# Kernel optimization log

Measured on AMD Instinct MI355X. Metric: run time of the kernel, lower is better.

## Reference

```python
import jax, jax.numpy as jnp
import numpy as np

N, FIN, HID, OUT, NC = 4096, 3000, 512, 64, 10


def _xavier(key, shape):
    b = (6.0 / (shape[0] + shape[1])) ** 0.5
    return jax.random.uniform(key, shape, minval=-b, maxval=b, dtype=jnp.float32)


def setup_inputs() -> dict:
    key = jax.random.key(0)
    ks = jax.random.split(key, 12)
    feat = jax.random.normal(ks[0], (N, FIN), jnp.float32)
    feat_a = jax.random.normal(ks[1], (N, FIN), jnp.float32)
    feat_mask = jax.random.normal(ks[2], (N, FIN), jnp.float32)
    adj = jax.random.uniform(ks[3], (N, N), jnp.float32)
    adj = adj / adj.sum(1, keepdims=True)  # row-normalized dense adjacency
    identify_matrix = jnp.eye(N, dtype=jnp.float32)
    graph_neigh = jnp.ones((N, N), jnp.float32)
    w2_1 = _xavier(ks[4], (FIN, HID))
    w2_2 = _xavier(ks[5], (HID, OUT))
    w2 = _xavier(ks[6], (OUT, FIN))
    lamda1 = jax.random.normal(ks[7], (N, 1), jnp.float32) * 0.5
    lamda2 = jax.random.normal(ks[8], (N, 1), jnp.float32) * 0.5
    cluster_w = _xavier(ks[9], (NC, OUT))
    cluster_b = jnp.zeros((NC,), jnp.float32)
    disc_w = _xavier(ks[10], (OUT, OUT)).reshape(1, OUT, OUT)
    disc_b = jnp.zeros((1,), jnp.float32)
    teacher_centers = jnp.zeros((1, OUT), jnp.float32)
    return dict(feat=feat, feat_a=feat_a, feat_mask=feat_mask, adj=adj,
                identify_matrix=identify_matrix, graph_neigh=graph_neigh,
                w2_1=w2_1, w2_2=w2_2, w2=w2, lamda1=lamda1, lamda2=lamda2,
                cluster_w=cluster_w, cluster_b=cluster_b, disc_w=disc_w,
                disc_b=disc_b, teacher_centers=teacher_centers)


def reference(feat, feat_a, feat_mask, adj, identify_matrix, graph_neigh,
              w2_1, w2_2, w2, lamda1, lamda2, cluster_w, cluster_b,
              disc_w, disc_b, teacher_centers):
    relu = jax.nn.relu

    def prop(z):
        # (lamda1 * I + lamda2 * adj) @ z  ==  lamda1 * z + lamda2 * (adj @ z)
        # (identify_matrix is the identity; row-scaling distributes over matmul)
        return lamda1 * z + lamda2 * jnp.matmul(adj, z)

    def branch(x):  # dropout is identity in eval mode
        z = relu(prop(jnp.matmul(x, w2_1)))
        return prop(jnp.matmul(z, w2_2))

    z = branch(feat)
    hiden_emb = z
    h = jnp.matmul(adj, jnp.matmul(z, w2))
    emb = relu(z)
    z_a = branch(feat_a)
    emb_a = relu(z_a)
    z_mask = branch(feat_mask)
    emb_mask = relu(z_mask)

    def readout(e):
        vsum = jnp.matmul(graph_neigh, e)
        g = vsum / graph_neigh.sum(1, keepdims=True)
        g = g / jnp.maximum(jnp.linalg.norm(g, axis=1, keepdims=True), 1e-12)
        return jax.nn.sigmoid(g)

    g, g_a, g_mask = readout(emb), readout(emb_a), readout(emb_mask)

    def disc(c, h_pl, h_mi):  # nn.Bilinear(n_h, n_h, 1); c broadcast to all rows
        sc1 = jnp.einsum('nd,ode,ne->no', h_pl, disc_w, c) + disc_b
        sc2 = jnp.einsum('nd,ode,ne->no', h_mi, disc_w, c) + disc_b
        return jnp.concatenate([sc1, sc2], axis=1)

    ret = disc(g, emb, emb_a)
    ret_a = disc(g_a, emb_a, emb)
    ret_mask = disc(g_mask, emb_mask, emb)

    c = jnp.matmul(z, cluster_w.T) + cluster_b
    c_mask = jnp.matmul(z_mask, cluster_w.T) + cluster_b

    def dino_loss(teacher, student):
        teacher = jax.lax.stop_gradient(teacher)
        sp = jax.nn.softmax(student / 0.9, axis=-1)
        tp = jax.nn.softmax((teacher - teacher_centers) / 0.06, axis=-1)
        return -(tp * jnp.log(sp + 1e-20)).sum(-1).mean()

    loss_mse = (dino_loss(z, z_mask) + dino_loss(z_mask, z)) / 2
    return (hiden_emb, h, ret, ret_a, ret_mask, c, c_mask, loss_mse)
```

## Files before the change

kernel.cpp:

```cpp
#include <hip/hip_runtime.h>
#include <math.h>


typedef __attribute__((ext_vector_type(8))) short bf16x8;
typedef __attribute__((ext_vector_type(4))) float f32x4;

__device__ inline ushort f2bf(float x) {
    unsigned u = __float_as_uint(x);
    return (ushort)((u + 0x7fffu + ((u >> 16) & 1u)) >> 16);
}
__device__ inline float bf2f(ushort h) { return __uint_as_float(((unsigned)h) << 16); }
__device__ inline int swzb(int row, int kb) {
    return ((row << 6) | kb) ^ ((row & 7) << 4);
}

struct SplitPtrs {
    const float*  A[3];
    const ushort* BTh[3];
    const ushort* BTl[3];
    const float*  Y[3];
    float*        C[3];
};

template<int EPI>
__global__ __launch_bounds__(256)
void gemm_mfma(SplitPtrs p, const float* __restrict__ l1, const float* __restrict__ l2,
               int K, int Kpad, int lda, int ldbt, int N) {
    const int zb = blockIdx.z;
    const float*  __restrict__ A   = p.A[zb];
    const ushort* __restrict__ BTh = p.BTh[zb];
    const ushort* __restrict__ BTl = p.BTl[zb];
    const float*  __restrict__ Y   = p.Y[zb];
    float* __restrict__ C = p.C[zb];

    const int tid  = threadIdx.x;
    const int lane = tid & 63;
    const int wave = tid >> 6;
    const int wm = wave >> 1, wn = wave & 1;
    const int lr = lane & 15, lg = lane >> 4;
    const int m0 = blockIdx.y * 128, n0 = blockIdx.x * 128;

    __shared__ ushort As[2][2][4096];
    __shared__ ushort Bs[2][2][4096];

    f32x4 acc[4][4];
#pragma unroll
    for (int i = 0; i < 4; ++i)
#pragma unroll
        for (int j = 0; j < 4; ++j) acc[i][j] = (f32x4){0.f, 0.f, 0.f, 0.f};

    int a_r[4], a_k[4];
#pragma unroll
    for (int p4 = 0; p4 < 4; ++p4) {
        int idx = tid + p4 * 256;
        a_r[p4] = idx >> 3; a_k[p4] = (idx & 7) * 4;
    }
    int b_n[2], b_k[2];
#pragma unroll
    for (int p2 = 0; p2 < 2; ++p2) {
        int idx = tid + p2 * 256;
        b_n[p2] = idx >> 2; b_k[p2] = (idx & 3) * 8;
    }

    float4 areg[4];
    uint4  bhreg[2], blreg[2];

    auto LOAD = [&](int k0) {
#pragma unroll
        for (int p4 = 0; p4 < 4; ++p4) {
            int k = k0 + a_k[p4];
            float4 v = make_float4(0.f, 0.f, 0.f, 0.f);
            if (k < K) v = *(const float4*)(A + (size_t)(m0 + a_r[p4]) * lda + k);
            areg[p4] = v;
        }
#pragma unroll
        for (int p2 = 0; p2 < 2; ++p2) {
            size_t off = (size_t)(n0 + b_n[p2]) * ldbt + k0 + b_k[p2];
            bhreg[p2] = *(const uint4*)(BTh + off);
            blreg[p2] = *(const uint4*)(BTl + off);
        }
    };
    auto WRITE = [&](int buf) {
#pragma unroll
        for (int p4 = 0; p4 < 4; ++p4) {
            float f[4] = {areg[p4].x, areg[p4].y, areg[p4].z, areg[p4].w};
            ushort h[4], l[4];
#pragma unroll
            for (int e = 0; e < 4; ++e) {
                h[e] = f2bf(f[e]);
                l[e] = f2bf(f[e] - bf2f(h[e]));
            }
            int off = swzb(a_r[p4], a_k[p4] * 2);
            *(uint2*)((char*)&As[buf][0][0] + off) =
                make_uint2((unsigned)h[0] | ((unsigned)h[1] << 16),
                           (unsigned)h[2] | ((unsigned)h[3] << 16));
            *(uint2*)((char*)&As[buf][1][0] + off) =
                make_uint2((unsigned)l[0] | ((unsigned)l[1] << 16),
                           (unsigned)l[2] | ((unsigned)l[3] << 16));
        }
#pragma unroll
        for (int p2 = 0; p2 < 2; ++p2) {
            int off = swzb(b_n[p2], b_k[p2] * 2);
            *(uint4*)((char*)&Bs[buf][0][0] + off) = bhreg[p2];
            *(uint4*)((char*)&Bs[buf][1][0] + off) = blreg[p2];
        }
    };

    LOAD(0);
    WRITE(0);
    const int nsteps = Kpad >> 5;
    for (int s = 0; s < nsteps; ++s) {
        const int cur = s & 1;
        if (s + 1 < nsteps) LOAD((s + 1) << 5);
        __syncthreads();
        bf16x8 af[2][4], bfr[2][4];
#pragma unroll
        for (int i = 0; i < 4; ++i) {
            int off = swzb(wm * 64 + i * 16 + lr, lg * 16);
            af[0][i] = *(const bf16x8*)((const char*)&As[cur][0][0] + off);
            af[1][i] = *(const bf16x8*)((const char*)&As[cur][1][0] + off);
        }
#pragma unroll
        for (int j = 0; j < 4; ++j) {
            int off = swzb(wn * 64 + j * 16 + lr, lg * 16);
            bfr[0][j] = *(const bf16x8*)((const char*)&Bs[cur][0][0] + off);
            bfr[1][j] = *(const bf16x8*)((const char*)&Bs[cur][1][0] + off);
        }
#pragma unroll
        for (int i = 0; i < 4; ++i)
#pragma unroll
            for (int j = 0; j < 4; ++j) {
                acc[i][j] = __builtin_amdgcn_mfma_f32_16x16x32_bf16(af[0][i], bfr[0][j], acc[i][j], 0, 0, 0);
                acc[i][j] = __builtin_amdgcn_mfma_f32_16x16x32_bf16(af[0][i], bfr[1][j], acc[i][j], 0, 0, 0);
                acc[i][j] = __builtin_amdgcn_mfma_f32_16x16x32_bf16(af[1][i], bfr[0][j], acc[i][j], 0, 0, 0);
            }
        if (s + 1 < nsteps) WRITE(cur ^ 1);
    }

#pragma unroll
    for (int i = 0; i < 4; ++i) {
#pragma unroll
        for (int r = 0; r < 4; ++r) {
            const int m = m0 + wm * 64 + i * 16 + lg * 4 + r;
            float L1 = 0.f, L2 = 0.f;
            if (EPI == 1) { L1 = l1[m]; L2 = l2[m]; }
#pragma unroll
            for (int j = 0; j < 4; ++j) {
                const int n = n0 + wn * 64 + j * 16 + lr;
                float v = acc[i][j][r];
                if (EPI == 1) {
                    float y = Y[(size_t)m * N + n];
                    v = fmaxf(L1 * y + L2 * v, 0.f);
                }
                C[(size_t)m * N + n] = v;
            }
        }
    }
}

__global__ __launch_bounds__(256)
void gemm_thin(const float* __restrict__ A, int lda,
               const ushort* __restrict__ BTh, const ushort* __restrict__ BTl, int ldbt,
               float* __restrict__ slab, int Mtot, int Nslab, int KC) {
    const int kc = blockIdx.x;
    const int m0 = blockIdx.y * 128;
    const int n0 = blockIdx.z * 64;
    const int tid = threadIdx.x;
    const int lane = tid & 63, wave = tid >> 6;
    const int lr = lane & 15, lg = lane >> 4;

    __shared__ ushort As[2][4096];
    __shared__ ushort Bs[2][2048];

    f32x4 acc[2][4];
#pragma unroll
    for (int i = 0; i < 2; ++i)
#pragma unroll
        for (int j = 0; j < 4; ++j) acc[i][j] = (f32x4){0.f, 0.f, 0.f, 0.f};

    const int kbeg = kc * KC;
    for (int k0 = kbeg; k0 < kbeg + KC; k0 += 32) {
#pragma unroll
        for (int p4 = 0; p4 < 4; ++p4) {
            int idx = tid + p4 * 256;
            int r = idx >> 3, kk = (idx & 7) * 4;
            float4 v = *(const float4*)(A + (size_t)(m0 + r) * lda + k0 + kk);
            float f[4] = {v.x, v.y, v.z, v.w};
            ushort h[4], l[4];
#pragma unroll
            for (int e = 0; e < 4; ++e) {
                h[e] = f2bf(f[e]);
                l[e] = f2bf(f[e] - bf2f(h[e]));
            }
            int off = swzb(r, kk * 2);
            *(uint2*)((char*)&As[0][0] + off) =
                make_uint2((unsigned)h[0] | ((unsigned)h[1] << 16),
                           (unsigned)h[2] | ((unsigned)h[3] << 16));
            *(uint2*)((char*)&As[1][0] + off) =
                make_uint2((unsigned)l[0] | ((unsigned)l[1] << 16),
                           (unsigned)l[2] | ((unsigned)l[3] << 16));
        }
        {
            int n = tid >> 2, kk8 = (tid & 3) * 8;
            size_t soff = (size_t)(n0 + n) * ldbt + k0 + kk8;
            int off = swzb(n, kk8 * 2);
            *(uint4*)((char*)&Bs[0][0] + off) = *(const uint4*)(BTh + soff);
            *(uint4*)((char*)&Bs[1][0] + off) = *(const uint4*)(BTl + soff);
        }
        __syncthreads();
        bf16x8 af[2][2], bfr[2][4];
#pragma unroll
        for (int i = 0; i < 2; ++i) {
            int off = swzb(wave * 32 + i * 16 + lr, lg * 16);
            af[0][i] = *(const bf16x8*)((const char*)&As[0][0] + off);
            af[1][i] = *(const bf16x8*)((const char*)&As[1][0] + off);
        }
#pragma unroll
        for (int j = 0; j < 4; ++j) {
            int off = swzb(j * 16 + lr, lg * 16);
            bfr[0][j] = *(const bf16x8*)((const char*)&Bs[0][0] + off);
            bfr[1][j] = *(const bf16x8*)((const char*)&Bs[1][0] + off);
        }
#pragma unroll
        for (int i = 0; i < 2; ++i)
#pragma unroll
            for (int j = 0; j < 4; ++j) {
                acc[i][j] = __builtin_amdgcn_mfma_f32_16x16x32_bf16(af[0][i], bfr[0][j], acc[i][j], 0, 0, 0);
                acc[i][j] = __builtin_amdgcn_mfma_f32_16x16x32_bf16(af[0][i], bfr[1][j], acc[i][j], 0, 0, 0);
                acc[i][j] = __builtin_amdgcn_mfma_f32_16x16x32_bf16(af[1][i], bfr[0][j], acc[i][j], 0, 0, 0);
            }
        __syncthreads();
    }

    float* out = slab + (size_t)kc * Mtot * Nslab;
#pragma unroll
    for (int i = 0; i < 2; ++i)
#pragma unroll
        for (int r = 0; r < 4; ++r) {
            const int m = m0 + wave * 32 + i * 16 + lg * 4 + r;
#pragma unroll
            for (int j = 0; j < 4; ++j) {
                const int n = n0 + j * 16 + lr;
                out[(size_t)m * Nslab + n] = acc[i][j][r];
            }
        }
}

__global__ void combine_sum(const float* __restrict__ slab, float* __restrict__ C,
                            int E, int nkc) {
    int e = (blockIdx.x * 256 + threadIdx.x) * 4;
    float4 s = make_float4(0.f, 0.f, 0.f, 0.f);
    for (int kc = 0; kc < nkc; ++kc) {
        float4 v = *(const float4*)(slab + (size_t)kc * E + e);
        s.x += v.x; s.y += v.y; s.z += v.z; s.w += v.w;
    }
    *(float4*)(C + e) = s;
}

struct ZOut { float* z[3]; };
__global__ void combine_g4(const float* __restrict__ slab, const float* __restrict__ y2,
                           const float* __restrict__ l1, const float* __restrict__ l2,
                           ZOut zo, int nkc) {
    int idx4 = blockIdx.x * 256 + threadIdx.x;
    int m = idx4 / 48;
    int n = (idx4 % 48) * 4;
    float4 s = make_float4(0.f, 0.f, 0.f, 0.f);
    for (int kc = 0; kc < nkc; ++kc) {
        float4 v = *(const float4*)(slab + (size_t)kc * 786432 + (size_t)m * 192 + n);
        s.x += v.x; s.y += v.y; s.z += v.z; s.w += v.w;
    }
    int b = n >> 6, d = n & 63;
    const float L1 = l1[m], L2 = l2[m];
    float4 y = *(const float4*)(y2 + (size_t)b * 262144 + (size_t)m * 64 + d);
    float4 r = make_float4(L1 * y.x + L2 * s.x, L1 * y.y + L2 * s.y,
                           L1 * y.z + L2 * s.z, L1 * y.w + L2 * s.w);
    *(float4*)(zo.z[b] + (size_t)m * 64 + d) = r;
}

__global__ __launch_bounds__(256)
void convT_split(const float* __restrict__ in, ushort* __restrict__ oh,
                 ushort* __restrict__ ol, int R, int C, int Ks) {
    __shared__ float t[64][65];
    const int r0 = blockIdx.x * 64, c0 = blockIdx.y * 64;
    const float* inz = in + (size_t)blockIdx.z * R * C;
    ushort* ohz = oh + (size_t)blockIdx.z * C * Ks;
    ushort* olz = ol + (size_t)blockIdx.z * C * Ks;
    const int tid = threadIdx.x;
#pragma unroll
    for (int pass = 0; pass < 16; ++pass) {
        int idx = tid + pass * 256;
        int r = idx >> 6, c = idx & 63;
        float v = 0.f;
        if (r0 + r < R) v = inz[(size_t)(r0 + r) * C + c0 + c];
        t[r][c] = v;
    }
    __syncthreads();
#pragma unroll
    for (int pass = 0; pass < 16; ++pass) {
        int idx = tid + pass * 256;
        int c = idx >> 6, r = idx & 63;
        float v = t[r][c];
        ushort h = f2bf(v);
        ushort l = f2bf(v - bf2f(h));
        size_t o = (size_t)(c0 + c) * Ks + r0 + r;
        ohz[o] = h; olz[o] = l;
    }
}

struct Ptrs3 {
    const float* A[3];
    const float* B[3];
    const float* Y[3];
    float*       C[3];
};

__global__ __launch_bounds__(256)
void gemm128(Ptrs3 p, int M, int N, int K) {
    const int zb = blockIdx.z;
    const float* __restrict__ A = p.A[zb];
    const float* __restrict__ B = p.B[zb];
    float* __restrict__ C = p.C[zb];

    const int tid = threadIdx.x;
    const int tm = tid >> 4, tn = tid & 15;
    const int m0 = blockIdx.y * 128, n0 = blockIdx.x * 128;

    __shared__ float As[16][132];
    __shared__ float Bs[16][132];

    float acc[2][2][4][4];
#pragma unroll
    for (int qi = 0; qi < 2; ++qi)
#pragma unroll
        for (int qj = 0; qj < 2; ++qj)
#pragma unroll
            for (int i = 0; i < 4; ++i)
#pragma unroll
                for (int j = 0; j < 4; ++j) acc[qi][qj][i][j] = 0.f;

    for (int k0 = 0; k0 < K; k0 += 16) {
        {
            int idx = tid * 4;
#pragma unroll
            for (int it = 0; it < 2; ++it, idx += 1024) {
                int r = idx >> 4, c = idx & 15;
                int k = k0 + c;
                const float* ap = A + (size_t)(m0 + r) * K + k;
                float4 v = make_float4(0.f, 0.f, 0.f, 0.f);
                if (k + 3 < K) {
                    v = *(const float4*)ap;
                } else {
                    if (k + 0 < K) v.x = ap[0];
                    if (k + 1 < K) v.y = ap[1];
                    if (k + 2 < K) v.z = ap[2];
                }
                As[c + 0][r] = v.x; As[c + 1][r] = v.y;
                As[c + 2][r] = v.z; As[c + 3][r] = v.w;
            }
        }
        {
            int idx = tid * 4;
#pragma unroll
            for (int it = 0; it < 2; ++it, idx += 1024) {
                int r = idx >> 7, c = idx & 127;
                int k = k0 + r, n = n0 + c;
                float4 v = make_float4(0.f, 0.f, 0.f, 0.f);
                if (k < K) {
                    const float* bp = B + (size_t)k * N + n;
                    if (n + 3 < N) {
                        v = *(const float4*)bp;
                    } else {
                        if (n + 0 < N) v.x = bp[0];
                        if (n + 1 < N) v.y = bp[1];
                        if (n + 2 < N) v.z = bp[2];
                    }
                }
                *(float4*)&Bs[r][c] = v;
            }
        }
        __syncthreads();

#pragma unroll
        for (int kk = 0; kk < 16; ++kk) {
            float4 a0 = *(const float4*)&As[kk][tm * 4];
            float4 a1 = *(const float4*)&As[kk][64 + tm * 4];
            float4 b0 = *(const float4*)&Bs[kk][tn * 4];
            float4 b1 = *(const float4*)&Bs[kk][64 + tn * 4];
            float a[2][4] = {{a0.x, a0.y, a0.z, a0.w}, {a1.x, a1.y, a1.z, a1.w}};
            float b[2][4] = {{b0.x, b0.y, b0.z, b0.w}, {b1.x, b1.y, b1.z, b1.w}};
#pragma unroll
            for (int qi = 0; qi < 2; ++qi)
#pragma unroll
                for (int qj = 0; qj < 2; ++qj)
#pragma unroll
                    for (int i = 0; i < 4; ++i)
#pragma unroll
                        for (int j = 0; j < 4; ++j)
                            acc[qi][qj][i][j] = fmaf(a[qi][i], b[qj][j], acc[qi][qj][i][j]);
        }
        __syncthreads();
    }

#pragma unroll
    for (int qi = 0; qi < 2; ++qi)
#pragma unroll
        for (int i = 0; i < 4; ++i) {
            const int m = m0 + qi * 64 + tm * 4 + i;
#pragma unroll
            for (int qj = 0; qj < 2; ++qj) {
                const int n = n0 + qj * 64 + tn * 4;
                float r[4] = {acc[qi][qj][i][0], acc[qi][qj][i][1],
                              acc[qi][qj][i][2], acc[qi][qj][i][3]};
                if (n + 3 < N) {
                    *(float4*)&C[(size_t)m * N + n] = make_float4(r[0], r[1], r[2], r[3]);
                } else {
#pragma unroll
                    for (int e = 0; e < 4; ++e)
                        if (n + e < N) C[(size_t)m * N + n + e] = r[e];
                }
            }
        }
}

__device__ inline float wsum64(float x) {
#pragma unroll
    for (int m = 32; m >= 1; m >>= 1) x += __shfl_xor(x, m);
    return x;
}
__device__ inline float wmax64(float x) {
#pragma unroll
    for (int m = 32; m >= 1; m >>= 1) x = fmaxf(x, __shfl_xor(x, m));
    return x;
}

__global__ void zero_small(float* gsum, float* loss) {
    int t = threadIdx.x;
    if (t < 192) gsum[t] = 0.f;
    if (t == 0) *loss = 0.f;
}

__global__ void colsum_relu(const float* __restrict__ z0,
                            const float* __restrict__ z1,
                            const float* __restrict__ z2,
                            float* __restrict__ gsum) {
    const float* z = blockIdx.y == 0 ? z0 : (blockIdx.y == 1 ? z1 : z2);
    int t = threadIdx.x;
    int col = t & 63, rq = t >> 6;
    int row0 = blockIdx.x * 128;
    float s = 0.f;
    for (int r = rq; r < 128; r += 4)
        s += fmaxf(z[(size_t)(row0 + r) * 64 + col], 0.f);
    __shared__ float red[4][64];
    red[rq][col] = s;
    __syncthreads();
    if (t < 64) {
        float tot = red[0][t] + red[1][t] + red[2][t] + red[3][t];
        atomicAdd(&gsum[blockIdx.y * 64 + t], tot);
    }
}

__global__ void finish_g(const float* __restrict__ gsum,
                         const float* __restrict__ disc_w,
                         float* __restrict__ v) {
    int d = threadIdx.x;
    __shared__ float g[64];
    for (int b = 0; b < 3; ++b) {
        float m = gsum[b * 64 + d] * (1.f / 4096.f);
        float nrm = sqrtf(wsum64(m * m));
        float den = fmaxf(nrm, 1e-12f);
        float gv = 1.f / (1.f + expf(-m / den));
        g[d] = gv;
        __syncthreads();
        float acc = 0.f;
        for (int e = 0; e < 64; ++e) acc += disc_w[d * 64 + e] * g[e];
        v[b * 64 + d] = acc;
        __syncthreads();
    }
}

__global__ void rows_kernel(const float* __restrict__ z,
                            const float* __restrict__ z_a,
                            const float* __restrict__ z_mask,
                            const float* __restrict__ v,
                            const float* __restrict__ disc_b,
                            const float* __restrict__ cw,
                            const float* __restrict__ cb,
                            const float* __restrict__ tc,
                            float* __restrict__ ret,
                            float* __restrict__ ret_a,
                            float* __restrict__ ret_mask,
                            float* __restrict__ c_out,
                            float* __restrict__ c_mask_out,
                            float* __restrict__ loss) {
    int wid = threadIdx.x >> 6;
    int lane = threadIdx.x & 63;
    int row = blockIdx.x * 4 + wid;
    size_t base = (size_t)row * 64 + lane;
    float zf = z[base], za = z_a[base], zm = z_mask[base];
    float ef = fmaxf(zf, 0.f), ea = fmaxf(za, 0.f), em = fmaxf(zm, 0.f);
    float v0 = v[lane], v1 = v[64 + lane], v2 = v[128 + lane];
    float db = disc_b[0];
    float s;
    s = wsum64(ef * v0); if (lane == 0) ret[row * 2 + 0] = s + db;
    s = wsum64(ea * v0); if (lane == 0) ret[row * 2 + 1] = s + db;
    s = wsum64(ea * v1); if (lane == 0) ret_a[row * 2 + 0] = s + db;
    s = wsum64(ef * v1); if (lane == 0) ret_a[row * 2 + 1] = s + db;
    s = wsum64(em * v2); if (lane == 0) ret_mask[row * 2 + 0] = s + db;
    s = wsum64(ef * v2); if (lane == 0) ret_mask[row * 2 + 1] = s + db;
#pragma unroll
    for (int k = 0; k < 10; ++k) {
        float w = cw[k * 64 + lane];
        s = wsum64(zf * w); if (lane == 0) c_out[row * 10 + k] = s + cb[k];
        s = wsum64(zm * w); if (lane == 0) c_mask_out[row * 10 + k] = s + cb[k];
    }
    float tcl = tc[lane];
    float l1v, l2v;
    {
        float x = zm * (1.f / 0.9f);
        float mx = wmax64(x); float pv = expf(x - mx); float sum = wsum64(pv);
        float sp = pv / sum;
        float xt = (zf - tcl) * (1.f / 0.06f);
        float mt = wmax64(xt); float pt = expf(xt - mt); float st = wsum64(pt);
        float tp = pt / st;
        l1v = -wsum64(tp * logf(sp + 1e-20f));
    }
    {
        float x = zf * (1.f / 0.9f);
        float mx = wmax64(x); float pv = expf(x - mx); float sum = wsum64(pv);
        float sp = pv / sum;
        float xt = (zm - tcl) * (1.f / 0.06f);
        float mt = wmax64(xt); float pt = expf(xt - mt); float st = wsum64(pt);
        float tp = pt / st;
        l2v = -wsum64(tp * logf(sp + 1e-20f));
    }
    if (lane == 0) atomicAdd(loss, (l1v + l2v) * (0.5f / 4096.f));
}

extern "C" void kernel_launch(void* const* d_in, const int* in_sizes, int n_in,
                              void* d_out, int out_size, void* d_ws, size_t ws_size,
                              hipStream_t stream) {
    (void)in_sizes; (void)n_in; (void)out_size; (void)ws_size;
    const float* feat   = (const float*)d_in[0];
    const float* feat_a = (const float*)d_in[1];
    const float* feat_m = (const float*)d_in[2];
    const float* adj    = (const float*)d_in[3];
    const float* w2_1   = (const float*)d_in[6];
    const float* w2_2   = (const float*)d_in[7];
    const float* w2     = (const float*)d_in[8];
    const float* l1     = (const float*)d_in[9];
    const float* l2     = (const float*)d_in[10];
    const float* cw     = (const float*)d_in[11];
    const float* cb     = (const float*)d_in[12];
    const float* dw     = (const float*)d_in[13];
    const float* dbv    = (const float*)d_in[14];
    const float* tc     = (const float*)d_in[15];

    float* out      = (float*)d_out;
    float* z_feat   = out;
    float* h_out    = out + 262144;
    float* ret      = out + 262144 + 12288000;
    float* ret_a    = ret + 8192;
    float* ret_mask = ret_a + 8192;
    float* c_out    = ret_mask + 8192;
    float* c_mask   = c_out + 40960;
    float* loss     = c_mask + 40960;

    float* ws = (float*)d_ws;
    size_t o = 0;
    float* y1   = ws + o; o += 6291456;
    float* z1   = ws + o; o += 6291456;
    float* y2   = ws + o; o += 786432;
    float* z_a  = ws + o; o += 262144;
    float* z_m  = ws + o; o += 262144;
    float* u    = ws + o; o += 262144;
    float* gsum = ws + o; o += 256;
    float* vv   = ws + o; o += 256;
    ushort* w21t_h = (ushort*)(ws + o); o += 770048;
    ushort* w21t_l = (ushort*)(ws + o); o += 770048;
    ushort* w22t_h = (ushort*)(ws + o); o += 16384;
    ushort* w22t_l = (ushort*)(ws + o); o += 16384;
    float* y1t_region = ws + o; o += 6291456;
    ushort* y1t_h  = (ushort*)y1t_region;
    ushort* y1t_l  = (ushort*)(y1t_region + 3145728);
    ushort* y2t_h  = (ushort*)y1t_region;
    ushort* y2t_l  = (ushort*)(y1t_region + 393216);
    ushort* zt_h   = (ushort*)(y1t_region + 786432);
    ushort* zt_l   = (ushort*)(y1t_region + 917504);
    float* slab = y1;

    zero_small<<<1, 256, 0, stream>>>(gsum, loss);

    convT_split<<<dim3(47, 8, 1), 256, 0, stream>>>(w2_1, w21t_h, w21t_l, 3000, 512, 3008);
    convT_split<<<dim3(8, 1, 1), 256, 0, stream>>>(w2_2, w22t_h, w22t_l, 512, 64, 512);

    SplitPtrs s1{};
    s1.A[0] = feat; s1.A[1] = feat_a; s1.A[2] = feat_m;
    s1.BTh[0] = s1.BTh[1] = s1.BTh[2] = w21t_h;
    s1.BTl[0] = s1.BTl[1] = s1.BTl[2] = w21t_l;
    s1.C[0] = y1; s1.C[1] = y1 + 2097152; s1.C[2] = y1 + 4194304;
    gemm_mfma<0><<<dim3(4, 32, 3), 256, 0, stream>>>(s1, nullptr, nullptr, 3000, 3008, 3000, 3008, 512);

    convT_split<<<dim3(64, 8, 3), 256, 0, stream>>>(y1, y1t_h, y1t_l, 4096, 512, 4096);

    SplitPtrs s2{};
    s2.A[0] = s2.A[1] = s2.A[2] = adj;
    s2.BTh[0] = y1t_h; s2.BTh[1] = y1t_h + 2097152; s2.BTh[2] = y1t_h + 4194304;
    s2.BTl[0] = y1t_l; s2.BTl[1] = y1t_l + 2097152; s2.BTl[2] = y1t_l + 4194304;
    s2.Y[0] = y1; s2.Y[1] = y1 + 2097152; s2.Y[2] = y1 + 4194304;
    s2.C[0] = z1; s2.C[1] = z1 + 2097152; s2.C[2] = z1 + 4194304;
    gemm_mfma<1><<<dim3(4, 32, 3), 256, 0, stream>>>(s2, l1, l2, 4096, 4096, 4096, 4096, 512);

    gemm_thin<<<dim3(2, 96, 1), 256, 0, stream>>>(z1, 512, w22t_h, w22t_l, 512,
                                                  slab, 12288, 64, 256);
    combine_sum<<<768, 256, 0, stream>>>(slab, y2, 786432, 2);

    convT_split<<<dim3(64, 1, 3), 256, 0, stream>>>(y2, y2t_h, y2t_l, 4096, 64, 4096);

    gemm_thin<<<dim3(8, 32, 3), 256, 0, stream>>>(adj, 4096, y2t_h, y2t_l, 4096,
                                                  slab, 4096, 192, 512);
    ZOut zo{}; zo.z[0] = z_feat; zo.z[1] = z_a; zo.z[2] = z_m;
    combine_g4<<<768, 256, 0, stream>>>(slab, y2, l1, l2, zo, 8);

    convT_split<<<dim3(64, 1, 1), 256, 0, stream>>>(z_feat, zt_h, zt_l, 4096, 64, 4096);

    gemm_thin<<<dim3(8, 32, 1), 256, 0, stream>>>(adj, 4096, zt_h, zt_l, 4096,
                                                  slab, 4096, 64, 512);
    combine_sum<<<256, 256, 0, stream>>>(slab, u, 262144, 8);

    Ptrs3 b6{};
    b6.A[0] = u; b6.B[0] = w2; b6.C[0] = h_out;
    gemm128<<<dim3(24, 32, 1), 256, 0, stream>>>(b6, 4096, 3000, 64);

    colsum_relu<<<dim3(32, 3), 256, 0, stream>>>(z_feat, z_a, z_m, gsum);
    finish_g<<<1, 64, 0, stream>>>(gsum, dw, vv);
    rows_kernel<<<1024, 256, 0, stream>>>(z_feat, z_a, z_m, vv, dbv, cw, cb, tc,
                                          ret, ret_a, ret_mask, c_out, c_mask, loss);
}
```

Baseline: 956.0 us.

## Narrow MFMA GEMM tiles to 128x64, single-buffer LDS, and route final GEMM through MFMA

The split-bf16 MFMA GEMM now uses 128x64 output tiles with a single LDS buffer instead of double buffering, which doubles the grid for the two large GEMMs so more blocks can be resident. The final u@w2 product now runs on the MFMA kernel with a pre-transposed split-bf16 w2 instead of the scalar FP32 gemm128, and convT_split gains column bounds checks to support this. The z1@w2_2 thin GEMM uses a finer K split with more partial slabs. In exchange, B-tile reuse per block drops and the single buffer adds an extra barrier per K step, reducing load/compute overlap.

```diff
diff --git a/kernel.cpp b/kernel.cpp
--- a/kernel.cpp
+++ b/kernel.cpp
@@ -38,16 +38,16 @@
     const int wave = tid >> 6;
     const int wm = wave >> 1, wn = wave & 1;
     const int lr = lane & 15, lg = lane >> 4;
-    const int m0 = blockIdx.y * 128, n0 = blockIdx.x * 128;
-
-    __shared__ ushort As[2][2][4096];
-    __shared__ ushort Bs[2][2][4096];
-
-    f32x4 acc[4][4];
+    const int m0 = blockIdx.y * 128, n0 = blockIdx.x * 64;
+
+    __shared__ ushort As[2][4096];
+    __shared__ ushort Bs[2][2048];
+
+    f32x4 acc[4][2];
 #pragma unroll
     for (int i = 0; i < 4; ++i)
 #pragma unroll
-        for (int j = 0; j < 4; ++j) acc[i][j] = (f32x4){0.f, 0.f, 0.f, 0.f};
+        for (int j = 0; j < 2; ++j) acc[i][j] = (f32x4){0.f, 0.f, 0.f, 0.f};
 
     int a_r[4], a_k[4];
 #pragma unroll
@@ -55,15 +55,10 @@
         int idx = tid + p4 * 256;
         a_r[p4] = idx >> 3; a_k[p4] = (idx & 7) * 4;
     }
-    int b_n[2], b_k[2];
-#pragma unroll
-    for (int p2 = 0; p2 < 2; ++p2) {
-        int idx = tid + p2 * 256;
-        b_n[p2] = idx >> 2; b_k[p2] = (idx & 3) * 8;
-    }
+    const int b_n = tid >> 2, b_k = (tid & 3) * 8;
 
     float4 areg[4];
-    uint4  bhreg[2], blreg[2];
+    uint4  bhreg, blreg;
 
     auto LOAD = [&](int k0) {
 #pragma unroll
@@ -73,14 +68,11 @@
             if (k < K) v = *(const float4*)(A + (size_t)(m0 + a_r[p4]) * lda + k);
             areg[p4] = v;
         }
-#pragma unroll
-        for (int p2 = 0; p2 < 2; ++p2) {
-            size_t off = (size_t)(n0 + b_n[p2]) * ldbt + k0 + b_k[p2];
-            bhreg[p2] = *(const uint4*)(BTh + off);
-            blreg[p2] = *(const uint4*)(BTl + off);
-        }
+        size_t off = (size_t)(n0 + b_n) * ldbt + k0 + b_k;
+        bhreg = *(const uint4*)(BTh + off);
+        blreg = *(const uint4*)(BTl + off);
     };
-    auto WRITE = [&](int buf) {
+    auto WRITE = [&]() {
 #pragma unroll
         for (int p4 = 0; p4 < 4; ++p4) {
             float f[4] = {areg[p4].x, areg[p4].y, areg[p4].z, areg[p4].w};
@@ -91,50 +83,46 @@
                 l[e] = f2bf(f[e] - bf2f(h[e]));
             }
             int off = swzb(a_r[p4], a_k[p4] * 2);
-            *(uint2*)((char*)&As[buf][0][0] + off) =
+            *(uint2*)((char*)&As[0][0] + off) =
                 make_uint2((unsigned)h[0] | ((unsigned)h[1] << 16),
                            (unsigned)h[2] | ((unsigned)h[3] << 16));
-            *(uint2*)((char*)&As[buf][1][0] + off) =
+            *(uint2*)((char*)&As[1][0] + off) =
                 make_uint2((unsigned)l[0] | ((unsigned)l[1] << 16),
                            (unsigned)l[2] | ((unsigned)l[3] << 16));
         }
-#pragma unroll
-        for (int p2 = 0; p2 < 2; ++p2) {
-            int off = swzb(b_n[p2], b_k[p2] * 2);
-            *(uint4*)((char*)&Bs[buf][0][0] + off) = bhreg[p2];
-            *(uint4*)((char*)&Bs[buf][1][0] + off) = blreg[p2];
-        }
+        int off = swzb(b_n, b_k * 2);
+        *(uint4*)((char*)&Bs[0][0] + off) = bhreg;
+        *(uint4*)((char*)&Bs[1][0] + off) = blreg;
     };
 
     LOAD(0);
-    WRITE(0);
     const int nsteps = Kpad >> 5;
     for (int s = 0; s < nsteps; ++s) {
-        const int cur = s & 1;
+        __syncthreads();
+        WRITE();
         if (s + 1 < nsteps) LOAD((s + 1) << 5);
         __syncthreads();
-        bf16x8 af[2][4], bfr[2][4];
+        bf16x8 af[2][4], bfr[2][2];
 #pragma unroll
         for (int i = 0; i < 4; ++i) {
             int off = swzb(wm * 64 + i * 16 + lr, lg * 16);
-            af[0][i] = *(const bf16x8*)((const char*)&As[cur][0][0] + off);
-            af[1][i] = *(const bf16x8*)((const char*)&As[cur][1][0] + off);
-        }
-#pragma unroll
-        for (int j = 0; j < 4; ++j) {
-            int off = swzb(wn * 64 + j * 16 + lr, lg * 16);
-            bfr[0][j] = *(const bf16x8*)((const char*)&Bs[cur][0][0] + off);
-            bfr[1][j] = *(const bf16x8*)((const char*)&Bs[cur][1][0] + off);
+            af[0][i] = *(const bf16x8*)((const char*)&As[0][0] + off);
+            af[1][i] = *(const bf16x8*)((const char*)&As[1][0] + off);
+        }
+#pragma unroll
+        for (int j = 0; j < 2; ++j) {
+            int off = swzb(wn * 32 + j * 16 + lr, lg * 16);
+            bfr[0][j] = *(const bf16x8*)((const char*)&Bs[0][0] + off);
+            bfr[1][j] = *(const bf16x8*)((const char*)&Bs[1][0] + off);
         }
 #pragma unroll
         for (int i = 0; i < 4; ++i)
 #pragma unroll
-            for (int j = 0; j < 4; ++j) {
+            for (int j = 0; j < 2; ++j) {
                 acc[i][j] = __builtin_amdgcn_mfma_f32_16x16x32_bf16(af[0][i], bfr[0][j], acc[i][j], 0, 0, 0);
                 acc[i][j] = __builtin_amdgcn_mfma_f32_16x16x32_bf16(af[0][i], bfr[1][j], acc[i][j], 0, 0, 0);
                 acc[i][j] = __builtin_amdgcn_mfma_f32_16x16x32_bf16(af[1][i], bfr[0][j], acc[i][j], 0, 0, 0);
             }
-        if (s + 1 < nsteps) WRITE(cur ^ 1);
     }
 
 #pragma unroll
@@ -145,14 +133,16 @@
             float L1 = 0.f, L2 = 0.f;
             if (EPI == 1) { L1 = l1[m]; L2 = l2[m]; }
 #pragma unroll
-            for (int j = 0; j < 4; ++j) {
-                const int n = n0 + wn * 64 + j * 16 + lr;
-                float v = acc[i][j][r];
-                if (EPI == 1) {
-                    float y = Y[(size_t)m * N + n];
-                    v = fmaxf(L1 * y + L2 * v, 0.f);
+            for (int j = 0; j < 2; ++j) {
+                const int n = n0 + wn * 32 + j * 16 + lr;
+                if (n < N) {
+                    float v = acc[i][j][r];
+                    if (EPI == 1) {
+                        float y = Y[(size_t)m * N + n];
+                        v = fmaxf(L1 * y + L2 * v, 0.f);
+                    }
+                    C[(size_t)m * N + n] = v;
                 }
-                C[(size_t)m * N + n] = v;
             }
         }
     }
@@ -291,7 +281,7 @@
         int idx = tid + pass * 256;
         int r = idx >> 6, c = idx & 63;
         float v = 0.f;
-        if (r0 + r < R) v = inz[(size_t)(r0 + r) * C + c0 + c];
+        if (r0 + r < R && c0 + c < C) v = inz[(size_t)(r0 + r) * C + c0 + c];
         t[r][c] = v;
     }
     __syncthreads();
@@ -299,127 +289,14 @@
     for (int pass = 0; pass < 16; ++pass) {
         int idx = tid + pass * 256;
         int c = idx >> 6, r = idx & 63;
-        float v = t[r][c];
-        ushort h = f2bf(v);
-        ushort l = f2bf(v - bf2f(h));
-        size_t o = (size_t)(c0 + c) * Ks + r0 + r;
-        ohz[o] = h; olz[o] = l;
-    }
-}
-
-struct Ptrs3 {
-    const float* A[3];
-    const float* B[3];
-    const float* Y[3];
-    float*       C[3];
-};
-
-__global__ __launch_bounds__(256)
-void gemm128(Ptrs3 p, int M, int N, int K) {
-    const int zb = blockIdx.z;
-    const float* __restrict__ A = p.A[zb];
-    const float* __restrict__ B = p.B[zb];
-    float* __restrict__ C = p.C[zb];
-
-    const int tid = threadIdx.x;
-    const int tm = tid >> 4, tn = tid & 15;
-    const int m0 = blockIdx.y * 128, n0 = blockIdx.x * 128;
-
-    __shared__ float As[16][132];
-    __shared__ float Bs[16][132];
-
-    float acc[2][2][4][4];
-#pragma unroll
-    for (int qi = 0; qi < 2; ++qi)
-#pragma unroll
-        for (int qj = 0; qj < 2; ++qj)
-#pragma unroll
-            for (int i = 0; i < 4; ++i)
-#pragma unroll
-                for (int j = 0; j < 4; ++j) acc[qi][qj][i][j] = 0.f;
-
-    for (int k0 = 0; k0 < K; k0 += 16) {
-        {
-            int idx = tid * 4;
-#pragma unroll
-            for (int it = 0; it < 2; ++it, idx += 1024) {
-                int r = idx >> 4, c = idx & 15;
-                int k = k0 + c;
-                const float* ap = A + (size_t)(m0 + r) * K + k;
-                float4 v = make_float4(0.f, 0.f, 0.f, 0.f);
-                if (k + 3 < K) {
-                    v = *(const float4*)ap;
-                } else {
-                    if (k + 0 < K) v.x = ap[0];
-                    if (k + 1 < K) v.y = ap[1];
-                    if (k + 2 < K) v.z = ap[2];
-                }
-                As[c + 0][r] = v.x; As[c + 1][r] = v.y;
-                As[c + 2][r] = v.z; As[c + 3][r] = v.w;
-            }
-        }
-        {
-            int idx = tid * 4;
-#pragma unroll
-            for (int it = 0; it < 2; ++it, idx += 1024) {
-                int r = idx >> 7, c = idx & 127;
-                int k = k0 + r, n = n0 + c;
-                float4 v = make_float4(0.f, 0.f, 0.f, 0.f);
-                if (k < K) {
-                    const float* bp = B + (size_t)k * N + n;
-                    if (n + 3 < N) {
-                        v = *(const float4*)bp;
-                    } else {
-                        if (n + 0 < N) v.x = bp[0];
-                        if (n + 1 < N) v.y = bp[1];
-                        if (n + 2 < N) v.z = bp[2];
-                    }
-                }
-                *(float4*)&Bs[r][c] = v;
-            }
-        }
-        __syncthreads();
-
-#pragma unroll
-        for (int kk = 0; kk < 16; ++kk) {
-            float4 a0 = *(const float4*)&As[kk][tm * 4];
-            float4 a1 = *(const float4*)&As[kk][64 + tm * 4];
-            float4 b0 = *(const float4*)&Bs[kk][tn * 4];
-            float4 b1 = *(const float4*)&Bs[kk][64 + tn * 4];
-            float a[2][4] = {{a0.x, a0.y, a0.z, a0.w}, {a1.x, a1.y, a1.z, a1.w}};
-            float b[2][4] = {{b0.x, b0.y, b0.z, b0.w}, {b1.x, b1.y, b1.z, b1.w}};
-#pragma unroll
-            for (int qi = 0; qi < 2; ++qi)
-#pragma unroll
-                for (int qj = 0; qj < 2; ++qj)
-#pragma unroll
-                    for (int i = 0; i < 4; ++i)
-#pragma unroll
-                        for (int j = 0; j < 4; ++j)
-                            acc[qi][qj][i][j] = fmaf(a[qi][i], b[qj][j], acc[qi][qj][i][j]);
-        }
-        __syncthreads();
-    }
-
-#pragma unroll
-    for (int qi = 0; qi < 2; ++qi)
-#pragma unroll
-        for (int i = 0; i < 4; ++i) {
-            const int m = m0 + qi * 64 + tm * 4 + i;
-#pragma unroll
-            for (int qj = 0; qj < 2; ++qj) {
-                const int n = n0 + qj * 64 + tn * 4;
-                float r[4] = {acc[qi][qj][i][0], acc[qi][qj][i][1],
-                              acc[qi][qj][i][2], acc[qi][qj][i][3]};
-                if (n + 3 < N) {
-                    *(float4*)&C[(size_t)m * N + n] = make_float4(r[0], r[1], r[2], r[3]);
-                } else {
-#pragma unroll
-                    for (int e = 0; e < 4; ++e)
-                        if (n + e < N) C[(size_t)m * N + n + e] = r[e];
-                }
-            }
-        }
+        if (c0 + c < C) {
+            float v = t[r][c];
+            ushort h = f2bf(v);
+            ushort l = f2bf(v - bf2f(h));
+            size_t o = (size_t)(c0 + c) * Ks + r0 + r;
+            ohz[o] = h; olz[o] = l;
+        }
+    }
 }
 
 __device__ inline float wsum64(float x) {
@@ -579,6 +456,8 @@
     ushort* w21t_l = (ushort*)(ws + o); o += 770048;
     ushort* w22t_h = (ushort*)(ws + o); o += 16384;
     ushort* w22t_l = (ushort*)(ws + o); o += 16384;
+    ushort* w2t_h  = (ushort*)(ws + o); o += 96256;
+    ushort* w2t_l  = (ushort*)(ws + o); o += 96256;
     float* y1t_region = ws + o; o += 6291456;
     ushort* y1t_h  = (ushort*)y1t_region;
     ushort* y1t_l  = (ushort*)(y1t_region + 3145728);
@@ -592,13 +471,14 @@
 
     convT_split<<<dim3(47, 8, 1), 256, 0, stream>>>(w2_1, w21t_h, w21t_l, 3000, 512, 3008);
     convT_split<<<dim3(8, 1, 1), 256, 0, stream>>>(w2_2, w22t_h, w22t_l, 512, 64, 512);
+    convT_split<<<dim3(1, 47, 1), 256, 0, stream>>>(w2, w2t_h, w2t_l, 64, 3000, 64);
 
     SplitPtrs s1{};
     s1.A[0] = feat; s1.A[1] = feat_a; s1.A[2] = feat_m;
     s1.BTh[0] = s1.BTh[1] = s1.BTh[2] = w21t_h;
     s1.BTl[0] = s1.BTl[1] = s1.BTl[2] = w21t_l;
     s1.C[0] = y1; s1.C[1] = y1 + 2097152; s1.C[2] = y1 + 4194304;
-    gemm_mfma<0><<<dim3(4, 32, 3), 256, 0, stream>>>(s1, nullptr, nullptr, 3000, 3008, 3000, 3008, 512);
+    gemm_mfma<0><<<dim3(8, 32, 3), 256, 0, stream>>>(s1, nullptr, nullptr, 3000, 3008, 3000, 3008, 512);
 
     convT_split<<<dim3(64, 8, 3), 256, 0, stream>>>(y1, y1t_h, y1t_l, 4096, 512, 4096);
 
@@ -608,11 +488,11 @@
     s2.BTl[0] = y1t_l; s2.BTl[1] = y1t_l + 2097152; s2.BTl[2] = y1t_l + 4194304;
     s2.Y[0] = y1; s2.Y[1] = y1 + 2097152; s2.Y[2] = y1 + 4194304;
     s2.C[0] = z1; s2.C[1] = z1 + 2097152; s2.C[2] = z1 + 4194304;
-    gemm_mfma<1><<<dim3(4, 32, 3), 256, 0, stream>>>(s2, l1, l2, 4096, 4096, 4096, 4096, 512);
-
-    gemm_thin<<<dim3(2, 96, 1), 256, 0, stream>>>(z1, 512, w22t_h, w22t_l, 512,
-                                                  slab, 12288, 64, 256);
-    combine_sum<<<768, 256, 0, stream>>>(slab, y2, 786432, 2);
+    gemm_mfma<1><<<dim3(8, 32, 3), 256, 0, stream>>>(s2, l1, l2, 4096, 4096, 4096, 4096, 512);
+
+    gemm_thin<<<dim3(4, 96, 1), 256, 0, stream>>>(z1, 512, w22t_h, w22t_l, 512,
+                                                  slab, 12288, 64, 128);
+    combine_sum<<<768, 256, 0, stream>>>(slab, y2, 786432, 4);
 
     convT_split<<<dim3(64, 1, 3), 256, 0, stream>>>(y2, y2t_h, y2t_l, 4096, 64, 4096);
 
@@ -627,9 +507,11 @@
                                                   slab, 4096, 64, 512);
     combine_sum<<<256, 256, 0, stream>>>(slab, u, 262144, 8);
 
-    Ptrs3 b6{};
-    b6.A[0] = u; b6.B[0] = w2; b6.C[0] = h_out;
-    gemm128<<<dim3(24, 32, 1), 256, 0, stream>>>(b6, 4096, 3000, 64);
+    SplitPtrs s6{};
+    s6.A[0] = u;
+    s6.BTh[0] = w2t_h; s6.BTl[0] = w2t_l;
+    s6.C[0] = h_out;
+    gemm_mfma<0><<<dim3(47, 32, 1), 256, 0, stream>>>(s6, nullptr, nullptr, 64, 64, 64, 64, 3000);
 
     colsum_relu<<<dim3(32, 3), 256, 0, stream>>>(z_feat, z_a, z_m, gsum);
     finish_g<<<1, 64, 0, stream>>>(gsum, dw, vv);
```

Result: faster. 921.8 us (-3.6%).
